# Performance work log

Hardware: AMD Instinct MI355X
Metric: run time of the kernel (lower is better)

## Reference

```python
import jax, jax.numpy as jnp
import numpy as np

B, T, D, H, L = 4, 2048, 256, 4, 2
HD = D // H
VOCAB, MAX_BITS, MLP_H = 32, 64, 64


def setup_inputs() -> dict:
    key = jax.random.key(0)
    ks = jax.random.split(key, 20)
    s = 0.02
    n = lambda k, shp: (jax.random.normal(k, shp, jnp.float32) * s)
    inp = {
        'tokens': jax.random.randint(ks[0], (B, T), 0, VOCAB),
        'embed': n(ks[1], (VOCAB, D)),
        'ln1_w': jnp.ones((L, D)), 'ln1_b': jnp.zeros((L, D)),
        'qkv_w': n(ks[2], (L, D, 3 * D)), 'qkv_b': jnp.zeros((L, 3 * D)),
        'proj_w': n(ks[3], (L, D, D)), 'proj_b': jnp.zeros((L, D)),
        'ln2_w': jnp.ones((L, D)), 'ln2_b': jnp.zeros((L, D)),
        'ffn1_w': n(ks[4], (L, D, 4 * D)), 'ffn1_b': jnp.zeros((L, 4 * D)),
        'ffn2_w': n(ks[5], (L, 4 * D, D)), 'ffn2_b': jnp.zeros((L, D)),
        'lnf_w': jnp.ones((D,)), 'lnf_b': jnp.zeros((D,)),
        'out_queries': n(ks[6], (MAX_BITS * 2, D)),
        'outp_w': n(ks[7], (D, 1)), 'outp_b': jnp.zeros((1,)),
        'mlp_w1': n(ks[8], (3, MLP_H)), 'mlp_b1': jnp.zeros((MLP_H,)),
        'mlp_w2': n(ks[9], (MLP_H, MLP_H)), 'mlp_b2': jnp.zeros((MLP_H,)),
        'mlp_w3': n(ks[10], (MLP_H, 2)), 'mlp_b3': jnp.zeros((2,)),
    }
    return inp


def _layernorm(x, w, b, eps=1e-5):
    mu = jnp.mean(x, axis=-1, keepdims=True)
    var = jnp.mean(jnp.square(x - mu), axis=-1, keepdims=True)
    return (x - mu) * jax.lax.rsqrt(var + eps) * w + b


def _rope_tables(t_len, hd):
    inv_freq = 1.0 / (10000.0 ** (jnp.arange(0, hd, 2, dtype=jnp.float32) / hd))
    freqs = jnp.outer(jnp.arange(t_len, dtype=jnp.float32), inv_freq)  # [T, hd/2]
    emb = jnp.concatenate([freqs, freqs], axis=-1)                     # [T, hd]
    return jnp.cos(emb)[None, :, None, :], jnp.sin(emb)[None, :, None, :]


def _rotate_half(x):
    x1, x2 = x[..., : x.shape[-1] // 2], x[..., x.shape[-1] // 2:]
    return jnp.concatenate([-x2, x1], axis=-1)


def _attention(x, qkv_w, qkv_b, proj_w, proj_b):
    b, t, c = x.shape
    qkv = (x @ qkv_w + qkv_b).reshape(b, t, 3, H, HD)
    q, k, v = qkv[:, :, 0], qkv[:, :, 1], qkv[:, :, 2]  # [B,T,H,HD]
    cos, sin = _rope_tables(t, HD)
    q = q * cos + _rotate_half(q) * sin
    k = k * cos + _rotate_half(k) * sin
    scores = jnp.einsum('bthd,bshd->bhts', q, k) / jnp.sqrt(jnp.float32(HD))
    causal = jnp.tril(jnp.ones((t, t), dtype=bool))
    scores = jnp.where(causal, scores, -jnp.inf)
    attn = jax.nn.softmax(scores, axis=-1)
    out = jnp.einsum('bhts,bshd->bthd', attn, v).reshape(b, t, c)
    return out @ proj_w + proj_b


def reference(tokens, embed, ln1_w, ln1_b, qkv_w, qkv_b, proj_w, proj_b,
              ln2_w, ln2_b, ffn1_w, ffn1_b, ffn2_w, ffn2_b, lnf_w, lnf_b,
              out_queries, outp_w, outp_b,
              mlp_w1, mlp_b1, mlp_w2, mlp_b2, mlp_w3, mlp_b3):
    x = embed[tokens]  # [B,T,D]
    for l in range(L):
        x = x + _attention(_layernorm(x, ln1_w[l], ln1_b[l]),
                           qkv_w[l], qkv_b[l], proj_w[l], proj_b[l])
        h = _layernorm(x, ln2_w[l], ln2_b[l])
        h = jax.nn.gelu(h @ ffn1_w[l] + ffn1_b[l], approximate=False)
        x = x + (h @ ffn2_w[l] + ffn2_b[l])
    x = _layernorm(x, lnf_w, lnf_b)
    # query cross-attention for bit-pair selection
    q_scores = jnp.einsum('qd,btd->bqt', out_queries, x) / jnp.sqrt(jnp.float32(D))
    q_attn = jax.nn.softmax(q_scores, axis=-1)           # [B, 2*MAX_BITS, T]
    selected = jnp.einsum('bqt,btd->bqd', q_attn, x)
    bits = jax.nn.sigmoid((selected @ outp_w + outp_b)[..., 0])
    pairs = bits.reshape(-1, MAX_BITS, 2)                # [B, MAX_BITS, 2]

    # sequential full-adder over bits
    def step(carry, ab):  # carry [B], ab [B,2]
        z = jnp.concatenate([ab, carry[:, None]], axis=-1)  # [B,3]
        h = jax.nn.relu(z @ mlp_w1 + mlp_b1)
        h = jax.nn.relu(h @ mlp_w2 + mlp_b2)
        o = jax.nn.sigmoid(h @ mlp_w3 + mlp_b3)
        return o[:, 1], o[:, 0]

    carry0 = jnp.zeros((pairs.shape[0],), jnp.float32)
    carry, sum_bits = jax.lax.scan(step, carry0, jnp.swapaxes(pairs, 0, 1))
    sum_all = jnp.concatenate([sum_bits.T, carry[:, None]], axis=1)  # [B, MAX_BITS+1]
    return sum_all, pairs, q_attn
```

## Files before the change

### kernel.cpp

```cpp
#include <hip/hip_runtime.h>
#include <hip/hip_bf16.h>

#define BB 4
#define TT 2048
#define DD 256
#define HH 4
#define HDD 64
#define NROW 8192
#define NQ 128

typedef __hip_bfloat16 bf16;
typedef __attribute__((ext_vector_type(8))) short bf8v;
typedef __attribute__((ext_vector_type(4))) short bf4v;
typedef __attribute__((ext_vector_type(4))) float f4v;
typedef __attribute__((ext_vector_type(2))) unsigned int u2v;

__device__ __forceinline__ bf16 f2b(float v){ return __float2bfloat16(v); }
__device__ __forceinline__ short f2bs(float v){
    bf16 h = __float2bfloat16(v);
    return *reinterpret_cast<short*>(&h);
}
__device__ __forceinline__ float bs2f(short s){
    bf16 h = *reinterpret_cast<bf16*>(&s);
    return __bfloat162float(h);
}
__device__ __forceinline__ float rl(float v, int l){
    return __uint_as_float(__builtin_amdgcn_readlane(__float_as_uint(v), l));
}

#define DPP_ROR_ADD(v, ctrl) \
    ((v) + __int_as_float(__builtin_amdgcn_update_dpp(0, __float_as_int(v), (ctrl), 0xF, 0xF, false)))
#define DPP_ROR_MAX(v, ctrl) \
    fmaxf((v), __int_as_float(__builtin_amdgcn_update_dpp(0, __float_as_int(v), (ctrl), 0xF, 0xF, false)))

__device__ __forceinline__ void plswap16(float v, float& a, float& b){
#if __has_builtin(__builtin_amdgcn_permlane16_swap)
    u2v r = __builtin_amdgcn_permlane16_swap(__float_as_uint(v), __float_as_uint(v), false, false);
    a = __uint_as_float(r.x); b = __uint_as_float(r.y);
#else
    a = v; b = v;
    asm volatile("" : "+v"(b));
    asm("v_permlane16_swap_b32 %0, %1" : "+v"(a), "+v"(b));
#endif
}
__device__ __forceinline__ void plswap32(float v, float& a, float& b){
#if __has_builtin(__builtin_amdgcn_permlane32_swap)
    u2v r = __builtin_amdgcn_permlane32_swap(__float_as_uint(v), __float_as_uint(v), false, false);
    a = __uint_as_float(r.x); b = __uint_as_float(r.y);
#else
    a = v; b = v;
    asm volatile("" : "+v"(b));
    asm("v_permlane32_swap_b32 %0, %1" : "+v"(a), "+v"(b));
#endif
}
__device__ __forceinline__ float swap16_add(float v){ float a,b; plswap16(v,a,b); return a + b; }
__device__ __forceinline__ float swap32_add(float v){ float a,b; plswap32(v,a,b); return a + b; }
__device__ __forceinline__ float swap16_max(float v){ float a,b; plswap16(v,a,b); return fmaxf(a,b); }
__device__ __forceinline__ float swap32_max(float v){ float a,b; plswap32(v,a,b); return fmaxf(a,b); }
__device__ __forceinline__ float wsum(float v){
    v = DPP_ROR_ADD(v, 0x121); v = DPP_ROR_ADD(v, 0x122);
    v = DPP_ROR_ADD(v, 0x124); v = DPP_ROR_ADD(v, 0x128);
    v = swap16_add(v); v = swap32_add(v);
    return v;
}
__device__ __forceinline__ float wmax(float v){
    v = DPP_ROR_MAX(v, 0x121); v = DPP_ROR_MAX(v, 0x122);
    v = DPP_ROR_MAX(v, 0x124); v = DPP_ROR_MAX(v, 0x128);
    v = swap16_max(v); v = swap32_max(v);
    return v;
}

#define MFMA32(A,B,C) __builtin_amdgcn_mfma_f32_16x16x32_bf16((A),(B),(C),0,0,0)
#if __has_builtin(__builtin_amdgcn_mfma_f32_16x16x16bf16_1k)
#define MFMA16(A,B,C) __builtin_amdgcn_mfma_f32_16x16x16bf16_1k((A),(B),(C),0,0,0)
#else
__device__ __forceinline__ f4v mfma16_asm(bf4v a, bf4v b, f4v c){
    f4v d;
    asm("v_mfma_f32_16x16x16_bf16 %0, %1, %2, %3" : "=v"(d) : "v"(a), "v"(b), "v"(c));
    return d;
}
#define MFMA16(A,B,C) mfma16_asm((A),(B),(C))
#endif

__global__ __launch_bounds__(256) void k_embln(const int* __restrict__ tok,
                                               const float* __restrict__ emb,
                                               const float* __restrict__ w,
                                               const float* __restrict__ b,
                                               float* __restrict__ x,
                                               bf16* __restrict__ Y){
    int row = blockIdx.x*4 + (threadIdx.x >> 6);
    int lane = threadIdx.x & 63;
    f4v v = *(const f4v*)(emb + (long)tok[row]*DD + lane*4);
    *(f4v*)(x + (long)row*DD + lane*4) = v;
    float s  = (v[0]+v[1]) + (v[2]+v[3]);
    float s2 = (v[0]*v[0]+v[1]*v[1]) + (v[2]*v[2]+v[3]*v[3]);
    s = wsum(s); s2 = wsum(s2);
    float mu  = s * (1.0f/DD);
    float var = s2 * (1.0f/DD) - mu*mu;
    float rs  = rsqrtf(var + 1e-5f);
    f4v wv4 = *(const f4v*)(w + lane*4);
    f4v bv4 = *(const f4v*)(b + lane*4);
    bf4v o;
    #pragma unroll
    for (int i=0;i<4;i++) o[i] = f2bs((v[i]-mu)*rs*wv4[i] + bv4[i]);
    *(bf4v*)(Y + (long)row*DD + lane*4) = o;
}

__global__ __launch_bounds__(256) void k_wtall(const float* __restrict__ qkvw,
                                               const float* __restrict__ projw,
                                               const float* __restrict__ f1w,
                                               const float* __restrict__ f2w,
                                               bf16* __restrict__ wt,
                                               const float* __restrict__ oq, bf16* __restrict__ oqb,
                                               float* __restrict__ cosT, float* __restrict__ sinT,
                                               const float* __restrict__ w2, float* __restrict__ w2t){
    __shared__ float t[32][33];
    int z = blockIdx.z;
    if (z == 8){
        int bid = blockIdx.y*32 + blockIdx.x;
        if (bid >= 256) return;
        int gid = bid*256 + threadIdx.y*32 + threadIdx.x;
        int tt = gid >> 5, dd = gid & 31;
        float invf = powf(10000.0f, -(float)(2*dd)/64.0f);
        float ang = (float)tt * invf;
        float sn, cs;
        sincosf(ang, &sn, &cs);
        cosT[gid] = cs; sinT[gid] = sn;
        if (gid < NQ*DD) oqb[gid] = f2b(oq[gid]);
        if (gid < 4096){ int j = gid >> 6, k = gid & 63; w2t[gid] = w2[k*64 + j]; }
        return;
    }
    int l = z >> 2, type = z & 3;
    long L = (long)l*786432;
    int K, M; const float* src; long doff;
    if (type == 0){ K=256;  M=768;  src = qkvw + (long)l*256*768;  doff = L; }
    else if (type == 1){ K=256;  M=256;  src = projw + (long)l*256*256; doff = L + 196608; }
    else if (type == 2){ K=256;  M=1024; src = f1w  + (long)l*256*1024; doff = L + 262144; }
    else               { K=1024; M=256;  src = f2w  + (long)l*1024*256; doff = L + 524288; }
    int m0 = blockIdx.x*32, k0 = blockIdx.y*32;
    if (m0 >= M || k0 >= K) return;
    bf16* dst = wt + doff;
    int tx = threadIdx.x, ty = threadIdx.y;
    #pragma unroll
    for (int i=0;i<4;i++)
        t[ty+i*8][tx] = src[(long)(k0+ty+i*8)*M + m0 + tx];
    __syncthreads();
    #pragma unroll
    for (int i=0;i<4;i++)
        dst[(long)(m0+ty+i*8)*K + k0 + tx] = f2b(t[tx][ty+i*8]);
}

__global__ __launch_bounds__(256) void k_lnb(const float* __restrict__ X,
                                             const float* __restrict__ w,
                                             const float* __restrict__ b,
                                             bf16* __restrict__ Y){
    int row = blockIdx.x*4 + (threadIdx.x >> 6);
    int lane = threadIdx.x & 63;
    f4v v = *(const f4v*)(X + (long)row*DD + lane*4);
    float s  = (v[0]+v[1]) + (v[2]+v[3]);
    float s2 = (v[0]*v[0]+v[1]*v[1]) + (v[2]*v[2]+v[3]*v[3]);
    s = wsum(s); s2 = wsum(s2);
    float mu  = s * (1.0f/DD);
    float var = s2 * (1.0f/DD) - mu*mu;
    float rs  = rsqrtf(var + 1e-5f);
    f4v wv4 = *(const f4v*)(w + lane*4);
    f4v bv4 = *(const f4v*)(b + lane*4);
    bf4v o;
    #pragma unroll
    for (int i=0;i<4;i++) o[i] = f2bs((v[i]-mu)*rs*wv4[i] + bv4[i]);
    *(bf4v*)(Y + (long)row*DD + lane*4) = o;
}

__global__ __launch_bounds__(256) void k_lnf(const float* __restrict__ X,
                                             const float* __restrict__ w,
                                             const float* __restrict__ b,
                                             const float* __restrict__ ow,
                                             bf16* __restrict__ Yb,
                                             float* __restrict__ g){
    int row = blockIdx.x*4 + (threadIdx.x >> 6);
    int lane = threadIdx.x & 63;
    f4v v = *(const f4v*)(X + (long)row*DD + lane*4);
    float s  = (v[0]+v[1]) + (v[2]+v[3]);
    float s2 = (v[0]*v[0]+v[1]*v[1]) + (v[2]*v[2]+v[3]*v[3]);
    s = wsum(s); s2 = wsum(s2);
    float mu  = s * (1.0f/DD);
    float var = s2 * (1.0f/DD) - mu*mu;
    float rs  = rsqrtf(var + 1e-5f);
    f4v wv4 = *(const f4v*)(w + lane*4);
    f4v bv4 = *(const f4v*)(b + lane*4);
    f4v ov4 = *(const f4v*)(ow + lane*4);
    bf4v o;
    float gp = 0.f;
    #pragma unroll
    for (int i=0;i<4;i++){
        float y = (v[i]-mu)*rs*wv4[i] + bv4[i];
        o[i] = f2bs(y);
        gp += y * ov4[i];
    }
    *(bf4v*)(Yb + (long)row*DD + lane*4) = o;
    gp = wsum(gp);
    if (lane == 0) g[row] = gp;
}

__global__ __launch_bounds__(256) void k_mgemm(const bf16* __restrict__ A,
                                               const bf16* __restrict__ Wt,
                                               const float* __restrict__ bias,
                                               float* __restrict__ Cf,
                                               bf16* __restrict__ Cb,
                                               int K, int M, int mode){
    __shared__ short As[2][128*64];
    __shared__ short Ws[2][64*64];
    int tid = threadIdx.x;
    int lane = tid & 63, wv = tid >> 6;
    int n0 = blockIdx.y * 128, m0 = blockIdx.x * 64;
    int rbase = (wv >> 1) * 64, cbase = (wv & 1) * 32;
    f4v acc[4][2] = {};
    bf8v va[4], vw[2];
    #pragma unroll
    for (int c=0;c<4;c++){
        int idx = c*256 + tid;
        va[c] = *(const bf8v*)(A + (long)(n0 + (idx>>3))*K + ((idx&7)<<3));
    }
    #pragma unroll
    for (int c=0;c<2;c++){
        int idx = c*256 + tid;
        vw[c] = *(const bf8v*)(Wt + (long)(m0 + (idx>>3))*K + ((idx&7)<<3));
    }
    int buf = 0;
    for (int k0 = 0; k0 < K; k0 += 64){
        #pragma unroll
        for (int c=0;c<4;c++){
            int idx = c*256 + tid, row = idx>>3;
            *(bf8v*)&As[buf][row*64 + (((idx&7)<<3) ^ ((row&7)<<3))] = va[c];
        }
        #pragma unroll
        for (int c=0;c<2;c++){
            int idx = c*256 + tid, row = idx>>3;
            *(bf8v*)&Ws[buf][row*64 + (((idx&7)<<3) ^ ((row&7)<<3))] = vw[c];
        }
        __syncthreads();
        if (k0 + 64 < K){
            #pragma unroll
            for (int c=0;c<4;c++){
                int idx = c*256 + tid;
                va[c] = *(const bf8v*)(A + (long)(n0 + (idx>>3))*K + k0 + 64 + ((idx&7)<<3));
            }
            #pragma unroll
            for (int c=0;c<2;c++){
                int idx = c*256 + tid;
                vw[c] = *(const bf8v*)(Wt + (long)(m0 + (idx>>3))*K + k0 + 64 + ((idx&7)<<3));
            }
        }
        int k8 = (lane >> 4) << 3;
        #pragma unroll
        for (int h=0; h<2; h++){
            bf8v af[4], bfr[2];
            #pragma unroll
            for (int i=0;i<4;i++){
                int row = rbase + i*16 + (lane&15);
                af[i] = *(bf8v*)&As[buf][row*64 + ((h*32 + k8) ^ ((row&7)<<3))];
            }
            #pragma unroll
            for (int j=0;j<2;j++){
                int row = cbase + j*16 + (lane&15);
                bfr[j] = *(bf8v*)&Ws[buf][row*64 + ((h*32 + k8) ^ ((row&7)<<3))];
            }
            #pragma unroll
            for (int i=0;i<4;i++)
                #pragma unroll
                for (int j=0;j<2;j++)
                    acc[i][j] = MFMA32(af[i], bfr[j], acc[i][j]);
        }
        buf ^= 1;
    }
    int rq = (lane >> 4) * 4;
    int cl = lane & 15;
    #pragma unroll
    for (int i=0;i<4;i++){
        #pragma unroll
        for (int j=0;j<2;j++){
            int m = m0 + cbase + j*16 + cl;
            float bs = bias[m];
            #pragma unroll
            for (int r=0;r<4;r++){
                int n = n0 + rbase + i*16 + rq + r;
                float v = acc[i][j][r] + bs;
                long idx = (long)n*M + m;
                if (mode == 0)      Cf[idx] = v;
                else if (mode == 1) Cf[idx] += v;
                else if (mode == 2) Cb[idx] = f2b(0.5f*v*(1.0f + erff(v*0.70710678118654752f)));
                else                Cb[idx] = f2b(v);
            }
        }
    }
}

__global__ __launch_bounds__(256) void k_mgemm64(const bf16* __restrict__ A,
                                                 const bf16* __restrict__ Wt,
                                                 const float* __restrict__ bias,
                                                 float* __restrict__ Cf,
                                                 bf16* __restrict__ Cb,
                                                 int K, int M, int mode){
    __shared__ short As[2][64*64];
    __shared__ short Ws[2][64*64];
    int tid = threadIdx.x;
    int lane = tid & 63, wv = tid >> 6;
    int n0 = blockIdx.y * 64, m0 = blockIdx.x * 64;
    int rbase = (wv >> 1) * 32, cbase = (wv & 1) * 32;
    f4v acc[2][2] = {};
    bf8v va[2], vw[2];
    #pragma unroll
    for (int c=0;c<2;c++){
        int idx = c*256 + tid;
        va[c] = *(const bf8v*)(A  + (long)(n0 + (idx>>3))*K + ((idx&7)<<3));
        vw[c] = *(const bf8v*)(Wt + (long)(m0 + (idx>>3))*K + ((idx&7)<<3));
    }
    int buf = 0;
    for (int k0 = 0; k0 < K; k0 += 64){
        #pragma unroll
        for (int c=0;c<2;c++){
            int idx = c*256 + tid, row = idx>>3;
            *(bf8v*)&As[buf][row*64 + (((idx&7)<<3) ^ ((row&7)<<3))] = va[c];
            *(bf8v*)&Ws[buf][row*64 + (((idx&7)<<3) ^ ((row&7)<<3))] = vw[c];
        }
        __syncthreads();
        if (k0 + 64 < K){
            #pragma unroll
            for (int c=0;c<2;c++){
                int idx = c*256 + tid;
                va[c] = *(const bf8v*)(A  + (long)(n0 + (idx>>3))*K + k0 + 64 + ((idx&7)<<3));
                vw[c] = *(const bf8v*)(Wt + (long)(m0 + (idx>>3))*K + k0 + 64 + ((idx&7)<<3));
            }
        }
        int k8 = (lane >> 4) << 3;
        #pragma unroll
        for (int h=0; h<2; h++){
            bf8v af[2], bfr[2];
            #pragma unroll
            for (int i=0;i<2;i++){
                int row = rbase + i*16 + (lane&15);
                af[i] = *(bf8v*)&As[buf][row*64 + ((h*32 + k8) ^ ((row&7)<<3))];
            }
            #pragma unroll
            for (int j=0;j<2;j++){
                int row = cbase + j*16 + (lane&15);
                bfr[j] = *(bf8v*)&Ws[buf][row*64 + ((h*32 + k8) ^ ((row&7)<<3))];
            }
            #pragma unroll
            for (int i=0;i<2;i++)
                #pragma unroll
                for (int j=0;j<2;j++)
                    acc[i][j] = MFMA32(af[i], bfr[j], acc[i][j]);
        }
        buf ^= 1;
    }
    int rq = (lane >> 4) * 4;
    int cl = lane & 15;
    #pragma unroll
    for (int i=0;i<2;i++){
        #pragma unroll
        for (int j=0;j<2;j++){
            int m = m0 + cbase + j*16 + cl;
            float bs = bias[m];
            #pragma unroll
            for (int r=0;r<4;r++){
                int n = n0 + rbase + i*16 + rq + r;
                float v = acc[i][j][r] + bs;
                long idx = (long)n*M + m;
                if (mode == 0)      Cf[idx] = v;
                else if (mode == 1) Cf[idx] += v;
                else if (mode == 2) Cb[idx] = f2b(0.5f*v*(1.0f + erff(v*0.70710678118654752f)));
                else                Cb[idx] = f2b(v);
            }
        }
    }
}

__global__ __launch_bounds__(256) void k_mgemmQKV(const bf16* __restrict__ A,
                                                  const bf16* __restrict__ Wt,
                                                  const float* __restrict__ bias,
                                                  const float* __restrict__ cosT,
                                                  const float* __restrict__ sinT,
                                                  bf16* __restrict__ qb,
                                                  bf16* __restrict__ kb,
                                                  bf16* __restrict__ vt){
    __shared__ short As[128*64];
    __shared__ short Ws[64*64];
    __shared__ short E[128][68];
    const int K = 256, M = 768;
    int tid = threadIdx.x;
    int lane = tid & 63, wv = tid >> 6;
    int n0 = blockIdx.y * 128, m0 = blockIdx.x * 64;
    int rbase = (wv >> 1) * 64, cbase = (wv & 1) * 32;
    f4v acc[4][2] = {};
    for (int k0 = 0; k0 < K; k0 += 64){
        bf8v va[4], vw[2];
        #pragma unroll
        for (int c=0;c<4;c++){
            int idx = c*256 + tid;
            va[c] = *(const bf8v*)(A + (long)(n0 + (idx>>3))*K + k0 + ((idx&7)<<3));
        }
        #pragma unroll
        for (int c=0;c<2;c++){
            int idx = c*256 + tid;
            vw[c] = *(const bf8v*)(Wt + (long)(m0 + (idx>>3))*K + k0 + ((idx&7)<<3));
        }
        __syncthreads();
        #pragma unroll
        for (int c=0;c<4;c++){
            int idx = c*256 + tid, row = idx>>3;
            *(bf8v*)&As[row*64 + (((idx&7)<<3) ^ ((row&7)<<3))] = va[c];
        }
        #pragma unroll
        for (int c=0;c<2;c++){
            int idx = c*256 + tid, row = idx>>3;
            *(bf8v*)&Ws[row*64 + (((idx&7)<<3) ^ ((row&7)<<3))] = vw[c];
        }
        __syncthreads();
        int k8 = (lane >> 4) << 3;
        #pragma unroll
        for (int h=0; h<2; h++){
            bf8v af[4], bfr[2];
            #pragma unroll
            for (int i=0;i<4;i++){
                int row = rbase + i*16 + (lane&15);
                af[i] = *(bf8v*)&As[row*64 + ((h*32 + k8) ^ ((row&7)<<3))];
            }
            #pragma unroll
            for (int j=0;j<2;j++){
                int row = cbase + j*16 + (lane&15);
                bfr[j] = *(bf8v*)&Ws[row*64 + ((h*32 + k8) ^ ((row&7)<<3))];
            }
            #pragma unroll
            for (int i=0;i<4;i++)
                #pragma unroll
                for (int j=0;j<2;j++)
                    acc[i][j] = MFMA32(af[i], bfr[j], acc[i][j]);
        }
    }
    int rq = (lane >> 4) * 4;
    int cl = lane & 15;
    #pragma unroll
    for (int i=0;i<4;i++){
        #pragma unroll
        for (int j=0;j<2;j++){
            int cc = cbase + j*16 + cl;
            float bs = bias[m0 + cc];
            #pragma unroll
            for (int r=0;r<4;r++)
                E[rbase + i*16 + rq + r][cc] = f2bs(acc[i][j][r] + bs);
        }
    }
    __syncthreads();
    int part = m0 >> 8;
    int h = (m0 >> 6) & 3;
    int b = n0 >> 11;
    int t0 = n0 & 2047;
    int bh = b*HH + h;
    if (part < 2){
        bf16* dst0 = part ? kb : qb;
        int r2 = tid >> 2;
        int c0 = (tid & 3) * 16;
        int cpx = c0 ^ 32;
        #pragma unroll
        for (int half=0; half<2; half++){
            int row = half*64 + r2;
            int t = t0 + row;
            bf8v e0 = *(bf8v*)&E[row][c0];
            bf8v e1 = *(bf8v*)&E[row][c0+8];
            bf8v p0 = *(bf8v*)&E[row][cpx];
            bf8v p1 = *(bf8v*)&E[row][cpx+8];
            const float* ct = cosT + t*32;
            const float* st = sinT + t*32;
            short o[16];
            #pragma unroll
            for (int i=0;i<8;i++){
                int d = c0 + i, dd = d & 31;
                float cs = ct[dd], sn = st[dd];
                float v = bs2f(e0[i]), v2 = bs2f(p0[i]);
                o[i] = f2bs((d < 32) ? (v*cs - v2*sn) : (v*cs + v2*sn));
            }
            #pragma unroll
            for (int i=0;i<8;i++){
                int d = c0 + 8 + i, dd = d & 31;
                float cs = ct[dd], sn = st[dd];
                float v = bs2f(e1[i]), v2 = bs2f(p1[i]);
                o[8+i] = f2bs((d < 32) ? (v*cs - v2*sn) : (v*cs + v2*sn));
            }
            short* dp = (short*)dst0 + ((long)bh*TT + t)*64 + c0;
            *(bf8v*)dp     = *(bf8v*)&o[0];
            *(bf8v*)(dp+8) = *(bf8v*)&o[8];
        }
    } else {
        int tIdx0 = t0 >> 6;
        int d  = (tid & 127) >> 1;
        int k0 = (tid & 1) * 32;
        int tt = tid >> 7;
        short o[32];
        #pragma unroll
        for (int k=0;k<32;k++) o[k] = E[tt*64 + k0 + k][d];
        short* dp = (short*)vt + (((long)bh*32 + tIdx0 + tt)*64 + d)*64 + k0;
        *(bf8v*)dp      = *(bf8v*)&o[0];
        *(bf8v*)(dp+8)  = *(bf8v*)&o[8];
        *(bf8v*)(dp+16) = *(bf8v*)&o[16];
        *(bf8v*)(dp+24) = *(bf8v*)&o[24];
    }
}

__global__ __launch_bounds__(256) void k_fattn(const bf16* __restrict__ qb,
                                               const bf16* __restrict__ kb,
                                               const bf16* __restrict__ vt,
                                               bf16* __restrict__ ob){
    __shared__ short Ks[2][64][72];
    __shared__ short Vs[2][64][68];
    int bh = blockIdx.y;
    int qt = (int)(gridDim.x - 1) - (int)blockIdx.x;
    int tid = threadIdx.x;
    int lane = tid & 63, w = tid >> 6;
    int col = lane & 15, quad = lane >> 4;
    int q0 = qt*64 + w*16;
    const bf16* qp = qb + ((long)bh*TT + q0 + col)*64 + quad*8;
    bf8v bq0 = *(const bf8v*)(qp);
    bf8v bq1 = *(const bf8v*)(qp + 32);
    f4v oc[4] = {};
    float lsum = 0.f;
    int qglob = q0 + col;
    int srow = tid >> 2, sc0 = (tid & 3) * 16;
    const short* kgb = (const short*)kb + ((long)bh*TT + srow)*64 + sc0;
    const short* vgb = (const short*)vt + (((long)bh*32)*64 + srow)*64 + sc0;

    bf8v pk0 = *(const bf8v*)kgb;
    bf8v pk1 = *(const bf8v*)(kgb + 8);
    bf8v pv0 = *(const bf8v*)vgb;
    bf8v pv1 = *(const bf8v*)(vgb + 8);
    *(bf8v*)&Ks[0][srow][sc0]     = pk0;
    *(bf8v*)&Ks[0][srow][sc0 + 8] = pk1;
    *(bf8v*)&Vs[0][srow][sc0]     = pv0;
    *(bf8v*)&Vs[0][srow][sc0 + 8] = pv1;

    int buf = 0;
    for (int kt=0; kt<=qt; kt++){
        __syncthreads();
        bool more = (kt < qt);
        if (more){
            const short* kg = kgb + (long)(kt+1)*4096;
            const short* vg = vgb + (long)(kt+1)*4096;
            pk0 = *(const bf8v*)kg;
            pk1 = *(const bf8v*)(kg + 8);
            pv0 = *(const bf8v*)vg;
            pv1 = *(const bf8v*)(vg + 8);
        }
        bool diag = (kt == qt);
        int ntmax = diag ? w : 3;
        bf4v bp[4];
        #pragma unroll
        for (int nt=0; nt<4; nt++){
            if (nt > ntmax) continue;
            bf8v ka0 = *(const bf8v*)&Ks[buf][nt*16 + col][quad*8];
            bf8v ka1 = *(const bf8v*)&Ks[buf][nt*16 + col][32 + quad*8];
            __builtin_amdgcn_s_setprio(1);
            f4v st = {};
            st = MFMA32(ka0, bq0, st);
            st = MFMA32(ka1, bq1, st);
            __builtin_amdgcn_s_setprio(0);
            int key0 = kt*64 + nt*16 + quad*4;
            bf4v pb;
            #pragma unroll
            for (int r=0; r<4; r++){
                float e = __expf(st[r]*0.125f);
                if (diag && (key0 + r > qglob)) e = 0.f;
                lsum += e;
                pb[r] = f2bs(e);
            }
            bp[nt] = pb;
        }
        __builtin_amdgcn_s_setprio(1);
        #pragma unroll
        for (int dt=0; dt<4; dt++){
            #pragma unroll
            for (int nt=0; nt<4; nt++){
                if (nt > ntmax) continue;
                bf4v va = *(const bf4v*)&Vs[buf][dt*16 + col][nt*16 + quad*4];
                oc[dt] = MFMA16(va, bp[nt], oc[dt]);
            }
        }
        __builtin_amdgcn_s_setprio(0);
        if (more){
            *(bf8v*)&Ks[buf^1][srow][sc0]     = pk0;
            *(bf8v*)&Ks[buf^1][srow][sc0 + 8] = pk1;
            *(bf8v*)&Vs[buf^1][srow][sc0]     = pv0;
            *(bf8v*)&Vs[buf^1][srow][sc0 + 8] = pv1;
        }
        buf ^= 1;
    }
    lsum += __shfl_xor(lsum, 16, 64);
    lsum += __shfl_xor(lsum, 32, 64);
    float linv = 1.0f / lsum;

    int b = bh / HH, h = bh % HH;
    long obase = ((long)b*TT + q0 + col)*DD + h*64 + quad*4;
    #pragma unroll
    for (int dt=0; dt<4; dt++){
        bf4v o4;
        #pragma unroll
        for (int r=0; r<4; r++) o4[r] = f2bs(oc[dt][r]*linv);
        *(bf4v*)(ob + obase + dt*16) = o4;
    }
}

__global__ __launch_bounds__(256) void k_score(const bf16* __restrict__ oqb,
                                               const bf16* __restrict__ xfb,
                                               float* __restrict__ S){
    int b = blockIdx.y, t0 = blockIdx.x*64;
    int tid = threadIdx.x, lane = tid & 63, w = tid >> 6;
    int col = lane & 15, quad = lane >> 4, k8 = quad << 3;
    const bf16* xb = xfb + (long)b*TT*DD;
    f4v acc[2][4] = {};
    #pragma unroll
    for (int ko=0; ko<8; ko++){
        int kk = ko*32 + k8;
        bf8v a0 = *(const bf8v*)(oqb + (long)(w*32 +      col)*DD + kk);
        bf8v a1 = *(const bf8v*)(oqb + (long)(w*32 + 16 + col)*DD + kk);
        #pragma unroll
        for (int bt=0; bt<4; bt++){
            bf8v bv = *(const bf8v*)(xb + (long)(t0 + bt*16 + col)*DD + kk);
            acc[0][bt] = MFMA32(a0, bv, acc[0][bt]);
            acc[1][bt] = MFMA32(a1, bv, acc[1][bt]);
        }
    }
    #pragma unroll
    for (int qt2=0; qt2<2; qt2++){
        #pragma unroll
        for (int bt=0; bt<4; bt++){
            #pragma unroll
            for (int r=0; r<4; r++){
                int q = w*32 + qt2*16 + quad*4 + r;
                S[((long)b*NQ + q)*TT + t0 + bt*16 + col] = acc[qt2][bt][r]*0.0625f;
            }
        }
    }
}

__global__ __launch_bounds__(256) void k_psoft(const float* __restrict__ S,
                                               const float* __restrict__ g,
                                               const float* __restrict__ obias,
                                               float* __restrict__ out_qattn,
                                               float* __restrict__ out_pairs,
                                               float* __restrict__ bits){
    __shared__ float cmax[4], cs[4], cg[4];
    int bq = blockIdx.x, b = bq >> 7;
    int tid = threadIdx.x, wv = tid >> 6, lane = tid & 63;
    const f4v* S4 = (const f4v*)(S + (long)bq*TT);
    f4v s0 = S4[tid], s1 = S4[tid + 256];
    float lmax = fmaxf(fmaxf(fmaxf(s0[0],s0[1]), fmaxf(s0[2],s0[3])),
                       fmaxf(fmaxf(s1[0],s1[1]), fmaxf(s1[2],s1[3])));
    lmax = wmax(lmax);
    if (lane == 0) cmax[wv] = lmax;
    __syncthreads();
    float m = fmaxf(fmaxf(cmax[0],cmax[1]), fmaxf(cmax[2],cmax[3]));
    const f4v* g4 = (const f4v*)(g + (long)b*TT);
    f4v gv0 = g4[tid], gv1 = g4[tid + 256];
    f4v e0, e1;
    #pragma unroll
    for (int i=0;i<4;i++){ e0[i] = __expf(s0[i]-m); e1[i] = __expf(s1[i]-m); }
    float lsum = (e0[0]+e0[1]+e0[2]+e0[3]) + (e1[0]+e1[1]+e1[2]+e1[3]);
    float gdot = (e0[0]*gv0[0]+e0[1]*gv0[1]+e0[2]*gv0[2]+e0[3]*gv0[3])
               + (e1[0]*gv1[0]+e1[1]*gv1[1]+e1[2]*gv1[2]+e1[3]*gv1[3]);
    lsum = wsum(lsum); gdot = wsum(gdot);
    if (lane == 0){ cs[wv] = lsum; cg[wv] = gdot; }
    __syncthreads();
    float Lr = (cs[0]+cs[1]) + (cs[2]+cs[3]);
    float G  = (cg[0]+cg[1]) + (cg[2]+cg[3]);
    float inv = 1.0f / Lr;
    f4v* out4 = (f4v*)(out_qattn + (long)bq*TT);
    out4[tid]       = e0 * inv;
    out4[tid + 256] = e1 * inv;
    if (tid == 0){
        float bit = 1.0f/(1.0f + expf(-(G*inv + obias[0])));
        bits[bq] = bit;
        out_pairs[bq] = bit;
    }
}

__global__ __launch_bounds__(64) void k_scan(const float* __restrict__ bits,
                                             const float* __restrict__ w1, const float* __restrict__ b1,
                                             const float* __restrict__ w2t, const float* __restrict__ b2,
                                             const float* __restrict__ w3, const float* __restrict__ b3,
                                             float* __restrict__ out_sum){
    __shared__ __align__(16) float h1s[2][64];
    int b = blockIdx.x, lane = threadIdx.x;
    float w1c0 = w1[lane], w1c1 = w1[64 + lane], w1c2 = w1[128 + lane];
    float b1v = b1[lane], b2v = b2[lane];
    float w3c0 = w3[lane*2 + 0], w3c1 = w3[lane*2 + 1];
    float b30 = b3[0], b31 = b3[1];
    const f4v* wrow = (const f4v*)(w2t + (long)lane*64);
    f4v c0v = wrow[0],  c1v = wrow[1],  c2v = wrow[2],  c3v = wrow[3],
        c4v = wrow[4],  c5v = wrow[5],  c6v = wrow[6],  c7v = wrow[7],
        c8v = wrow[8],  c9v = wrow[9],  cav = wrow[10], cbv = wrow[11],
        ccv = wrow[12], cdv = wrow[13], cev = wrow[14], cfv = wrow[15];
    float z0v = bits[b*128 + lane*2 + 0];
    float z1v = bits[b*128 + lane*2 + 1];
    float carry = 0.f;
    float a1 = rl(z0v, 0)*w1c0 + rl(z1v, 0)*w1c1 + b1v;
    for (int step=0; step<64; step++){
        float h1 = fmaxf(carry*w1c2 + a1, 0.f);
        float* hb = h1s[step & 1];
        hb[lane] = h1;
        __syncthreads();
        if (step < 63){
            a1 = rl(z0v, step+1)*w1c0 + rl(z1v, step+1)*w1c1 + b1v;
        }
        const f4v* hv = (const f4v*)hb;
        f4v va = hv[0]*c0v,  vb = hv[1]*c1v,  vc = hv[2]*c2v,   vd = hv[3]*c3v;
        va += hv[4]*c4v;   vb += hv[5]*c5v;   vc += hv[6]*c6v;   vd += hv[7]*c7v;
        va += hv[8]*c8v;   vb += hv[9]*c9v;   vc += hv[10]*cav;  vd += hv[11]*cbv;
        va += hv[12]*ccv;  vb += hv[13]*cdv;  vc += hv[14]*cev;  vd += hv[15]*cfv;
        f4v vs = (va + vb) + (vc + vd);
        float h2 = fmaxf(((vs[0] + vs[1]) + (vs[2] + vs[3])) + b2v, 0.f);
        float t0 = h2*w3c0, t1 = h2*w3c1;
        t0 = DPP_ROR_ADD(t0, 0x121); t1 = DPP_ROR_ADD(t1, 0x121);
        t0 = DPP_ROR_ADD(t0, 0x122); t1 = DPP_ROR_ADD(t1, 0x122);
        t0 = DPP_ROR_ADD(t0, 0x124); t1 = DPP_ROR_ADD(t1, 0x124);
        t0 = DPP_ROR_ADD(t0, 0x128); t1 = DPP_ROR_ADD(t1, 0x128);
        t0 = swap16_add(t0); t1 = swap16_add(t1);
        t0 = swap32_add(t0); t1 = swap32_add(t1);
        float o0 = 1.0f/(1.0f + __expf(-(t0 + b30)));
        carry    = 1.0f/(1.0f + __expf(-(t1 + b31)));
        if (lane == 0) out_sum[b*65 + step] = o0;
    }
    if (lane == 0) out_sum[b*65 + 64] = carry;
}

extern "C" void kernel_launch(void* const* d_in, const int* in_sizes, int n_in,
                              void* d_out, int out_size, void* d_ws, size_t ws_size,
                              hipStream_t stream){
    const int*   tok   = (const int*)d_in[0];
    const float* emb   = (const float*)d_in[1];
    const float* ln1w  = (const float*)d_in[2];
    const float* ln1b  = (const float*)d_in[3];
    const float* qkvw  = (const float*)d_in[4];
    const float* qkvb  = (const float*)d_in[5];
    const float* projw = (const float*)d_in[6];
    const float* projb = (const float*)d_in[7];
    const float* ln2w  = (const float*)d_in[8];
    const float* ln2b  = (const float*)d_in[9];
    const float* f1w   = (const float*)d_in[10];
    const float* f1b   = (const float*)d_in[11];
    const float* f2w   = (const float*)d_in[12];
    const float* f2bb  = (const float*)d_in[13];
    const float* lnfw  = (const float*)d_in[14];
    const float* lnfb  = (const float*)d_in[15];
    const float* oq    = (const float*)d_in[16];
    const float* ow    = (const float*)d_in[17];
    const float* obias = (const float*)d_in[18];
    const float* w1    = (const float*)d_in[19];
    const float* b1    = (const float*)d_in[20];
    const float* w2    = (const float*)d_in[21];
    const float* b2    = (const float*)d_in[22];
    const float* w3    = (const float*)d_in[23];
    const float* b3    = (const float*)d_in[24];
    float* out = (float*)d_out;

    const long MB = 1048576;
    char* W = (char*)d_ws;
    float* x     = (float*)(W);
    bf16*  attnb = (bf16*)(W + 8*MB);
    bf16*  hb    = (bf16*)(W + 16*MB);
    bf16*  qb    = (bf16*)(W + 32*MB);
    bf16*  kb    = (bf16*)(W + 36*MB);
    bf16*  vt    = (bf16*)(W + 44*MB);
    bf16*  xnb   = (bf16*)(W + 48*MB);
    bf16*  wt    = (bf16*)(W + 52*MB);
    float* bits  = (float*)(W + 55*MB);
    bf16*  oqb   = (bf16*)(W + 56*MB);
    float* cosT  = (float*)(W + 57*MB);
    float* sinT  = cosT + 65536;
    float* w2t   = (float*)(W + 58*MB);
    bf16*  xfb   = (bf16*)(W + 32*MB);
    float* g     = (float*)(W + 36*MB);
    float* S     = (float*)(W + 40*MB);

    k_wtall<<<dim3(32, 32, 9), dim3(32,8), 0, stream>>>(qkvw, projw, f1w, f2w, wt,
                                                        oq, oqb, cosT, sinT, w2, w2t);

    k_embln<<<NROW/4, 256, 0, stream>>>(tok, emb, ln1w, ln1b, x, xnb);
    for (int l=0; l<2; l++){
        long L = (long)l*786432;
        if (l) k_lnb<<<NROW/4, 256, 0, stream>>>(x, ln1w + l*DD, ln1b + l*DD, xnb);
        k_mgemmQKV<<<dim3(768/64, 64), 256, 0, stream>>>(
            xnb, wt + L, qkvb + l*768, cosT, sinT, qb, kb, vt);
        k_fattn<<<dim3(TT/64, BB*HH), 256, 0, stream>>>(qb, kb, vt, attnb);
        k_mgemm64<<<dim3(256/64, NROW/64), 256, 0, stream>>>(
            attnb, wt + L + 196608, projb + l*DD, x, (bf16*)0, 256, 256, 1);
        k_lnb<<<NROW/4, 256, 0, stream>>>(x, ln2w + l*DD, ln2b + l*DD, xnb);
        k_mgemm<<<dim3(1024/64, 64), 256, 0, stream>>>(
            xnb, wt + L + 262144, f1b + l*1024, (float*)0, hb, 256, 1024, 2);
        k_mgemm64<<<dim3(256/64, NROW/64), 256, 0, stream>>>(
            hb, wt + L + 524288, f2bb + l*DD, x, (bf16*)0, 1024, 256, 1);
    }
    k_lnf<<<NROW/4, 256, 0, stream>>>(x, lnfw, lnfb, ow, xfb, g);
    k_score<<<dim3(TT/64, BB), 256, 0, stream>>>(oqb, xfb, S);
    k_psoft<<<BB*NQ, 256, 0, stream>>>(S, g, obias, out + 772, out + 260, bits);
    k_scan<<<4, 64, 0, stream>>>(bits, w1, b1, w2t, b2, w3, b3, out);
}
```

Baseline: 365.5 us.

## Process two query tiles per wave in flash attention; shrink score tiles

The attention kernel now runs 128 threads (2 waves), and each wave handles two 16-row query groups that share the same K/V fragments read from shared memory. This halves LDS reads of K and V per query row and doubles per-wave MFMA work, at the cost of more registers and fewer waves per block. The score kernel halves its time tile per block to launch twice as many blocks, aiming for better occupancy on the small final GEMM.

```diff
diff --git a/kernel.cpp b/kernel.cpp
--- a/kernel.cpp
+++ b/kernel.cpp
@@ -507,7 +507,7 @@
     }
 }
 
-__global__ __launch_bounds__(256) void k_fattn(const bf16* __restrict__ qb,
+__global__ __launch_bounds__(128) void k_fattn(const bf16* __restrict__ qb,
                                                const bf16* __restrict__ kb,
                                                const bf16* __restrict__ vt,
                                                bf16* __restrict__ ob){
@@ -518,25 +518,37 @@
     int tid = threadIdx.x;
     int lane = tid & 63, w = tid >> 6;
     int col = lane & 15, quad = lane >> 4;
-    int q0 = qt*64 + w*16;
-    const bf16* qp = qb + ((long)bh*TT + q0 + col)*64 + quad*8;
-    bf8v bq0 = *(const bf8v*)(qp);
-    bf8v bq1 = *(const bf8v*)(qp + 32);
-    f4v oc[4] = {};
-    float lsum = 0.f;
-    int qglob = q0 + col;
-    int srow = tid >> 2, sc0 = (tid & 3) * 16;
+    int q0A = qt*64 + w*16;
+    int q0B = q0A + 32;
+    const bf16* qpA = qb + ((long)bh*TT + q0A + col)*64 + quad*8;
+    const bf16* qpB = qb + ((long)bh*TT + q0B + col)*64 + quad*8;
+    bf8v bqA0 = *(const bf8v*)(qpA);
+    bf8v bqA1 = *(const bf8v*)(qpA + 32);
+    bf8v bqB0 = *(const bf8v*)(qpB);
+    bf8v bqB1 = *(const bf8v*)(qpB + 32);
+    f4v ocA[4] = {}, ocB[4] = {};
+    float lsumA = 0.f, lsumB = 0.f;
+    int qgA = q0A + col, qgB = q0B + col;
+    int srow = tid >> 1, sc0 = (tid & 1) * 32;
     const short* kgb = (const short*)kb + ((long)bh*TT + srow)*64 + sc0;
     const short* vgb = (const short*)vt + (((long)bh*32)*64 + srow)*64 + sc0;
 
-    bf8v pk0 = *(const bf8v*)kgb;
+    bf8v pk0 = *(const bf8v*)(kgb);
     bf8v pk1 = *(const bf8v*)(kgb + 8);
-    bf8v pv0 = *(const bf8v*)vgb;
+    bf8v pk2 = *(const bf8v*)(kgb + 16);
+    bf8v pk3 = *(const bf8v*)(kgb + 24);
+    bf8v pv0 = *(const bf8v*)(vgb);
     bf8v pv1 = *(const bf8v*)(vgb + 8);
-    *(bf8v*)&Ks[0][srow][sc0]     = pk0;
-    *(bf8v*)&Ks[0][srow][sc0 + 8] = pk1;
-    *(bf8v*)&Vs[0][srow][sc0]     = pv0;
-    *(bf8v*)&Vs[0][srow][sc0 + 8] = pv1;
+    bf8v pv2 = *(const bf8v*)(vgb + 16);
+    bf8v pv3 = *(const bf8v*)(vgb + 24);
+    *(bf8v*)&Ks[0][srow][sc0]      = pk0;
+    *(bf8v*)&Ks[0][srow][sc0 + 8]  = pk1;
+    *(bf8v*)&Ks[0][srow][sc0 + 16] = pk2;
+    *(bf8v*)&Ks[0][srow][sc0 + 24] = pk3;
+    *(bf8v*)&Vs[0][srow][sc0]      = pv0;
+    *(bf8v*)&Vs[0][srow][sc0 + 8]  = pv1;
+    *(bf8v*)&Vs[0][srow][sc0 + 16] = pv2;
+    *(bf8v*)&Vs[0][srow][sc0 + 24] = pv3;
 
     int buf = 0;
     for (int kt=0; kt<=qt; kt++){
@@ -545,84 +557,116 @@
         if (more){
             const short* kg = kgb + (long)(kt+1)*4096;
             const short* vg = vgb + (long)(kt+1)*4096;
-            pk0 = *(const bf8v*)kg;
-            pk1 = *(const bf8v*)(kg + 8);
-            pv0 = *(const bf8v*)vg;
-            pv1 = *(const bf8v*)(vg + 8);
+            pk0 = *(const bf8v*)(kg);      pk1 = *(const bf8v*)(kg + 8);
+            pk2 = *(const bf8v*)(kg + 16); pk3 = *(const bf8v*)(kg + 24);
+            pv0 = *(const bf8v*)(vg);      pv1 = *(const bf8v*)(vg + 8);
+            pv2 = *(const bf8v*)(vg + 16); pv3 = *(const bf8v*)(vg + 24);
         }
         bool diag = (kt == qt);
-        int ntmax = diag ? w : 3;
-        bf4v bp[4];
+        int ntA = diag ? w : 3;
+        int ntB = diag ? 2 + w : 3;
+        bf4v bpA[4], bpB[4];
         #pragma unroll
         for (int nt=0; nt<4; nt++){
-            if (nt > ntmax) continue;
+            if (nt > ntB) continue;
             bf8v ka0 = *(const bf8v*)&Ks[buf][nt*16 + col][quad*8];
             bf8v ka1 = *(const bf8v*)&Ks[buf][nt*16 + col][32 + quad*8];
-            __builtin_amdgcn_s_setprio(1);
-            f4v st = {};
-            st = MFMA32(ka0, bq0, st);
-            st = MFMA32(ka1, bq1, st);
-            __builtin_amdgcn_s_setprio(0);
             int key0 = kt*64 + nt*16 + quad*4;
-            bf4v pb;
-            #pragma unroll
-            for (int r=0; r<4; r++){
-                float e = __expf(st[r]*0.125f);
-                if (diag && (key0 + r > qglob)) e = 0.f;
-                lsum += e;
-                pb[r] = f2bs(e);
-            }
-            bp[nt] = pb;
+            if (nt <= ntA){
+                __builtin_amdgcn_s_setprio(1);
+                f4v st = {};
+                st = MFMA32(ka0, bqA0, st);
+                st = MFMA32(ka1, bqA1, st);
+                __builtin_amdgcn_s_setprio(0);
+                bf4v pb;
+                #pragma unroll
+                for (int r=0; r<4; r++){
+                    float e = __expf(st[r]*0.125f);
+                    if (diag && (key0 + r > qgA)) e = 0.f;
+                    lsumA += e;
+                    pb[r] = f2bs(e);
+                }
+                bpA[nt] = pb;
+            }
+            {
+                __builtin_amdgcn_s_setprio(1);
+                f4v st = {};
+                st = MFMA32(ka0, bqB0, st);
+                st = MFMA32(ka1, bqB1, st);
+                __builtin_amdgcn_s_setprio(0);
+                bf4v pb;
+                #pragma unroll
+                for (int r=0; r<4; r++){
+                    float e = __expf(st[r]*0.125f);
+                    if (diag && (key0 + r > qgB)) e = 0.f;
+                    lsumB += e;
+                    pb[r] = f2bs(e);
+                }
+                bpB[nt] = pb;
+            }
         }
         __builtin_amdgcn_s_setprio(1);
         #pragma unroll
         for (int dt=0; dt<4; dt++){
             #pragma unroll
             for (int nt=0; nt<4; nt++){
-                if (nt > ntmax) continue;
+                if (nt > ntB) continue;
                 bf4v va = *(const bf4v*)&Vs[buf][dt*16 + col][nt*16 + quad*4];
-                oc[dt] = MFMA16(va, bp[nt], oc[dt]);
+                if (nt <= ntA) ocA[dt] = MFMA16(va, bpA[nt], ocA[dt]);
+                ocB[dt] = MFMA16(va, bpB[nt], ocB[dt]);
             }
         }
         __builtin_amdgcn_s_setprio(0);
         if (more){
-            *(bf8v*)&Ks[buf^1][srow][sc0]     = pk0;
-            *(bf8v*)&Ks[buf^1][srow][sc0 + 8] = pk1;
-            *(bf8v*)&Vs[buf^1][srow][sc0]     = pv0;
-            *(bf8v*)&Vs[buf^1][srow][sc0 + 8] = pv1;
+            *(bf8v*)&Ks[buf^1][srow][sc0]      = pk0;
+            *(bf8v*)&Ks[buf^1][srow][sc0 + 8]  = pk1;
+            *(bf8v*)&Ks[buf^1][srow][sc0 + 16] = pk2;
+            *(bf8v*)&Ks[buf^1][srow][sc0 + 24] = pk3;
+            *(bf8v*)&Vs[buf^1][srow][sc0]      = pv0;
+            *(bf8v*)&Vs[buf^1][srow][sc0 + 8]  = pv1;
+            *(bf8v*)&Vs[buf^1][srow][sc0 + 16] = pv2;
+            *(bf8v*)&Vs[buf^1][srow][sc0 + 24] = pv3;
         }
         buf ^= 1;
     }
-    lsum += __shfl_xor(lsum, 16, 64);
-    lsum += __shfl_xor(lsum, 32, 64);
-    float linv = 1.0f / lsum;
+    lsumA += __shfl_xor(lsumA, 16, 64);
+    lsumA += __shfl_xor(lsumA, 32, 64);
+    lsumB += __shfl_xor(lsumB, 16, 64);
+    lsumB += __shfl_xor(lsumB, 32, 64);
+    float linvA = 1.0f / lsumA;
+    float linvB = 1.0f / lsumB;
 
     int b = bh / HH, h = bh % HH;
-    long obase = ((long)b*TT + q0 + col)*DD + h*64 + quad*4;
+    long obaseA = ((long)b*TT + q0A + col)*DD + h*64 + quad*4;
+    long obaseB = ((long)b*TT + q0B + col)*DD + h*64 + quad*4;
     #pragma unroll
     for (int dt=0; dt<4; dt++){
-        bf4v o4;
-        #pragma unroll
-        for (int r=0; r<4; r++) o4[r] = f2bs(oc[dt][r]*linv);
-        *(bf4v*)(ob + obase + dt*16) = o4;
+        bf4v o4A, o4B;
+        #pragma unroll
+        for (int r=0; r<4; r++){
+            o4A[r] = f2bs(ocA[dt][r]*linvA);
+            o4B[r] = f2bs(ocB[dt][r]*linvB);
+        }
+        *(bf4v*)(ob + obaseA + dt*16) = o4A;
+        *(bf4v*)(ob + obaseB + dt*16) = o4B;
     }
 }
 
 __global__ __launch_bounds__(256) void k_score(const bf16* __restrict__ oqb,
                                                const bf16* __restrict__ xfb,
                                                float* __restrict__ S){
-    int b = blockIdx.y, t0 = blockIdx.x*64;
+    int b = blockIdx.y, t0 = blockIdx.x*32;
     int tid = threadIdx.x, lane = tid & 63, w = tid >> 6;
     int col = lane & 15, quad = lane >> 4, k8 = quad << 3;
     const bf16* xb = xfb + (long)b*TT*DD;
-    f4v acc[2][4] = {};
+    f4v acc[2][2] = {};
     #pragma unroll
     for (int ko=0; ko<8; ko++){
         int kk = ko*32 + k8;
         bf8v a0 = *(const bf8v*)(oqb + (long)(w*32 +      col)*DD + kk);
         bf8v a1 = *(const bf8v*)(oqb + (long)(w*32 + 16 + col)*DD + kk);
         #pragma unroll
-        for (int bt=0; bt<4; bt++){
+        for (int bt=0; bt<2; bt++){
             bf8v bv = *(const bf8v*)(xb + (long)(t0 + bt*16 + col)*DD + kk);
             acc[0][bt] = MFMA32(a0, bv, acc[0][bt]);
             acc[1][bt] = MFMA32(a1, bv, acc[1][bt]);
@@ -631,7 +675,7 @@
     #pragma unroll
     for (int qt2=0; qt2<2; qt2++){
         #pragma unroll
-        for (int bt=0; bt<4; bt++){
+        for (int bt=0; bt<2; bt++){
             #pragma unroll
             for (int r=0; r<4; r++){
                 int q = w*32 + qt2*16 + quad*4 + r;
@@ -789,7 +833,7 @@
         if (l) k_lnb<<<NROW/4, 256, 0, stream>>>(x, ln1w + l*DD, ln1b + l*DD, xnb);
         k_mgemmQKV<<<dim3(768/64, 64), 256, 0, stream>>>(
             xnb, wt + L, qkvb + l*768, cosT, sinT, qb, kb, vt);
-        k_fattn<<<dim3(TT/64, BB*HH), 256, 0, stream>>>(qb, kb, vt, attnb);
+        k_fattn<<<dim3(TT/64, BB*HH), 128, 0, stream>>>(qb, kb, vt, attnb);
         k_mgemm64<<<dim3(256/64, NROW/64), 256, 0, stream>>>(
             attnb, wt + L + 196608, projb + l*DD, x, (bf16*)0, 256, 256, 1);
         k_lnb<<<NROW/4, 256, 0, stream>>>(x, ln2w + l*DD, ln2b + l*DD, xnb);
@@ -799,7 +843,7 @@
             hb, wt + L + 524288, f2bb + l*DD, x, (bf16*)0, 1024, 256, 1);
     }
     k_lnf<<<NROW/4, 256, 0, stream>>>(x, lnfw, lnfb, ow, xfb, g);
-    k_score<<<dim3(TT/64, BB), 256, 0, stream>>>(oqb, xfb, S);
+    k_score<<<dim3(TT/32, BB), 256, 0, stream>>>(oqb, xfb, S);
     k_psoft<<<BB*NQ, 256, 0, stream>>>(S, g, obias, out + 772, out + 260, bits);
     k_scan<<<4, 64, 0, stream>>>(bits, w1, b1, w2t, b2, w3, b3, out);
 }
```

Measured after the change: 395.1 us. 8.1% more time.
